# Kernel tuning notes

Measured on AMD Instinct MI355X. Metric: run time of the kernel, lower is better.

The kernel has to match this reference:

```python
import jax, jax.numpy as jnp
import numpy as np


def _c1(x, W, b):
    # 1x1 conv: W [out,in], x [B,in,H,W]
    return jnp.einsum('oi,bihw->bohw', W, x) + b[None, :, None, None]


def _c3(x, W, b):
    # 3x3 conv, stride 1, padding 1 (SAME)
    y = jax.lax.conv_general_dilated(x, W, (1, 1), 'SAME',
                                     dimension_numbers=('NCHW', 'OIHW', 'NCHW'))
    return y + b[None, :, None, None]


def _resize(x, h, w):
    # matches torch F.interpolate(mode='bilinear', align_corners=False)
    return jax.image.resize(x, (x.shape[0], x.shape[1], h, w), 'linear', antialias=False)


def setup_inputs() -> dict:
    key = jax.random.key(0)
    ks = jax.random.split(key, 20)
    B, C, H, W = 4, 64, 128, 128
    d = C // 8

    def n(k, shape, s=0.05):
        return jax.random.normal(k, shape, dtype=jnp.float32) * s

    z = lambda c: jnp.zeros((c,), jnp.float32)
    return {
        'x': jax.random.normal(ks[0], (B, C, H, W), dtype=jnp.float32),
        'mask': jax.random.normal(ks[1], (B, 64, H, W), dtype=jnp.float32),
        'Wq': n(ks[2], (d, C)), 'bq': z(d),
        'Wk': n(ks[3], (d, C)), 'bk': z(d),
        'Wv': n(ks[4], (C, C)), 'bv': z(C),
        'alpha1': jax.random.uniform(ks[5], (1,), dtype=jnp.float32),
        'alpha2': jax.random.uniform(ks[6], (1,), dtype=jnp.float32),
        'mq_w1': n(ks[7], (64, 64, 3, 3)), 'mq_b1': z(64),
        'mq_w2': n(ks[8], (d, 64)), 'mq_b2': z(d),
        'mk_w1': n(ks[9], (64, 64, 3, 3)), 'mk_b1': z(64),
        'mk_w2': n(ks[10], (d, 64)), 'mk_b2': z(d),
        'ca_w1': n(ks[11], (64, 64)), 'ca_b1': z(64),
        'ca_w2': n(ks[12], (64, 64)), 'ca_b2': z(64),
    }


def reference(x, mask, Wq, bq, Wk, bk, Wv, bv, alpha1, alpha2,
              mq_w1, mq_b1, mq_w2, mq_b2, mk_w1, mk_b1, mk_w2, mk_b2,
              ca_w1, ca_b1, ca_w2, ca_b2):
    B, C, H, W = x.shape
    h2, w2 = H // 2, W // 2
    N = h2 * w2

    mask_q = _c1(jax.nn.relu(_c3(mask, mq_w1, mq_b1)), mq_w2, mq_b2)
    mask_k = _c1(jax.nn.relu(_c3(mask, mk_w1, mk_b1)), mk_w2, mk_b2)
    xq = _c1(x, Wq, bq)  # [B, d, H, W]
    xk = _c1(x, Wk, bk)

    pq = mask_q * xq * alpha1 + xq * (1.0 - alpha1)
    pq = _resize(pq, h2, w2).reshape(B, -1, N)          # [B, d, N]
    pk = mask_k * xk * alpha2 + xk * (1.0 - alpha2)
    pk = _resize(pk, h2, w2).reshape(B, -1, N)          # [B, d, N]

    energy = jnp.einsum('bdn,bdm->bnm', pq, pk)         # [B, N, N]
    attn = jax.nn.softmax(energy, axis=-1)

    pv = _resize(_c1(x, Wv, bv), h2, w2).reshape(B, C, N)
    out = jnp.einsum('bcn,bmn->bcm', pv, attn)          # value @ attn^T
    out = out.reshape(B, C, h2, w2)
    out = _resize(out, H, W)
    out = _c1(jax.nn.relu(_c1(out, ca_w1, ca_b1)), ca_w2, ca_b2)
    return out + x
```

## Files before the change

kernel.cpp:

```cpp
#include <hip/hip_runtime.h>
#include <hip/hip_bf16.h>

typedef _Float16 half8 __attribute__((ext_vector_type(8)));
typedef _Float16 half4v __attribute__((ext_vector_type(4)));
typedef _Float16 half2v __attribute__((ext_vector_type(2)));
typedef __fp16 pkh2 __attribute__((ext_vector_type(2)));
typedef float f32x4 __attribute__((ext_vector_type(4)));

static __device__ __forceinline__ f32x4 mfma16(half8 a, half8 b, f32x4 c) {
    return __builtin_amdgcn_mfma_f32_16x16x32_f16(a, b, c, 0, 0, 0);
}

typedef const __attribute__((address_space(1))) unsigned int* gas_ptr;
typedef __attribute__((address_space(3))) unsigned int* las_ptr;
static __device__ __forceinline__ void gload16(const void* g, void* l) {
    __builtin_amdgcn_global_load_lds((gas_ptr)g, (las_ptr)l, 16, 0, 0);
}

static __device__ __forceinline__ half2v cvt2(float a, float b) {
    pkh2 t = __builtin_amdgcn_cvt_pkrtz(a, b);
    return __builtin_bit_cast(half2v, t);
}
static __device__ __forceinline__ half8 pk8(f32x4 a, f32x4 b) {
    half2v x0 = cvt2(a[0], a[1]);
    half2v x1 = cvt2(a[2], a[3]);
    half2v x2 = cvt2(b[0], b[1]);
    half2v x3 = cvt2(b[2], b[3]);
    half4v lo = __builtin_shufflevector(x0, x1, 0, 1, 2, 3);
    half4v hi = __builtin_shufflevector(x2, x3, 0, 1, 2, 3);
    return __builtin_shufflevector(lo, hi, 0, 1, 2, 3, 4, 5, 6, 7);
}
static __device__ __forceinline__ half4v pk4(f32x4 a) {
    half2v x0 = cvt2(a[0], a[1]);
    half2v x1 = cvt2(a[2], a[3]);
    return __builtin_shufflevector(x0, x1, 0, 1, 2, 3);
}

#define WS_APCONV   0u
#define WS_APW2S    147456u
#define WS_APCA     151552u
#define WS_APW2K4   159744u
#define WS_PACKED   196608u
#define WS_MASKQ    8849408u
#define WS_MASKK    10946560u
#define WS_Q16      13043712u
#define WS_K16      13305856u
#define WS_V16      13568000u
#define WS_ZB       15665152u
#define WS_PACC8    17762304u
#define WS_PML8     34539520u
#define WS_END8     35063808u
#define WS_PACC4    WS_PACKED
#define WS_PML4     WS_MASKQ

__global__ __launch_bounds__(256) void prep_pack_kernel(
    const float* __restrict__ mask,
    const float* __restrict__ mqw1, const float* __restrict__ mkw1,
    const float* __restrict__ mqw2, const float* __restrict__ mkw2,
    const float* __restrict__ caw1, const float* __restrict__ caw2,
    _Float16* __restrict__ packed,
    _Float16* __restrict__ ApackConv, _Float16* __restrict__ ApackW2s,
    _Float16* __restrict__ ApackCA, _Float16* __restrict__ ApackW2K4)
{
    int tid = threadIdx.x;
    if (blockIdx.z < 4) {
        int ich = blockIdx.y, b = blockIdx.z;
        _Float16* Pb = packed + ((size_t)b * 8 + ich) * 130 * 130 * 8;
        if (blockIdx.x < 2) {
            for (int p = blockIdx.x * 260 + tid; p < (int)(blockIdx.x + 1) * 260; p += 256) {
                int row, col;
                if (p < 130)      { row = 0;       col = p; }
                else if (p < 260) { row = 129;     col = p - 130; }
                else if (p < 390) { row = p - 260; col = 0; }
                else              { row = p - 390; col = 129; }
                half8 z = {};
                *(half8*)(Pb + ((size_t)row * 130 + col) * 8) = z;
            }
        }
        int x = tid & 127;
        int sy = blockIdx.x * 2 + (tid >> 7);
        half8 v;
#pragma unroll
        for (int cc = 0; cc < 8; cc++)
            v[cc] = (_Float16)mask[(((size_t)(b * 64 + ich * 8 + cc)) * 128 + sy) * 128 + x];
        *(half8*)(Pb + (((size_t)(sy + 1)) * 130 + (x + 1)) * 8) = v;
        return;
    }
    int tid0 = (blockIdx.y * 64 + blockIdx.x) * 256 + tid;
    const int stride = 512 * 256;
    for (int idx = tid0; idx < 73728; idx += stride) {
        int j = idx & 7, lane = (idx >> 3) & 63, mf = (idx >> 9) & 3;
        int ks18 = idx >> 11;
        int br = ks18 / 18, kstep = ks18 % 18;
        int oc = mf * 16 + (lane & 15);
        int g = lane >> 4;
        int k = kstep * 32 + g * 8 + j;
        int tap = k >> 6, ic = k & 63;
        int dy = tap / 3, dx = tap - dy * 3;
        const float* w1 = br ? mkw1 : mqw1;
        ApackConv[idx] = (_Float16)w1[((oc * 64 + ic) * 3 + dy) * 3 + dx];
    }
    for (int idx = tid0; idx < 2048; idx += stride) {
        int j = idx & 7, lane = (idx >> 3) & 63;
        int f = (idx >> 9) & 1, br = idx >> 10;
        int dc = lane & 15, g = lane >> 4;
        int kap = 16 * (2 * f + (j >> 2)) + 4 * g + (j & 3);
        const float* w2 = br ? mkw2 : mqw2;
        ApackW2s[idx] = (_Float16)((dc < 8) ? w2[dc * 64 + kap] : 0.f);
    }
    for (int idx = tid0; idx < 4096; idx += stride) {
        int j = idx & 7, lane = (idx >> 3) & 63, mf = (idx >> 9) & 3, f = idx >> 11;
        int cp = mf * 16 + (lane & 15), g = lane >> 4;
        int kap = 16 * (2 * f + (j >> 2)) + 4 * g + (j & 3);
        ApackCA[idx] = (_Float16)caw1[cp * 64 + kap];
    }
    for (int idx = tid0; idx < 4096; idx += stride) {
        int j = idx & 7, lane = (idx >> 3) & 63, mf = (idx >> 9) & 3, f = idx >> 11;
        int cc = mf * 16 + (lane & 15), g = lane >> 4;
        int cpk = f * 32 + g * 8 + j;
        ApackW2K4[idx] = (_Float16)caw2[cc * 64 + cpk];
    }
}

__global__ __launch_bounds__(256) void conv_mask_kernel(
    const _Float16* __restrict__ packed,
    const _Float16* __restrict__ ApackConv,
    const _Float16* __restrict__ ApackW2s,
    const float* __restrict__ mqb1, const float* __restrict__ mqb2,
    const float* __restrict__ mkb1, const float* __restrict__ mkb2,
    float* __restrict__ maskq, float* __restrict__ maskk)
{
    __shared__ __align__(16) _Float16 S[8 * 4 * 72 * 8];
    int tid = threadIdx.x;
    int lane = tid & 63, w = tid >> 6;
    int x0 = blockIdx.x * 64;
    int y0 = blockIdx.y * 2;
    int b = blockIdx.z;
    int row = w & 1, br = w >> 1;
    int q = lane & 15, g = lane >> 4;

    const _Float16* Pb = packed + (size_t)b * 8 * 130 * 130 * 8;
#pragma unroll
    for (int i = 0; i < 8; i++) {
        int p = w * 8 + i;
        int ich = p >> 2, pr = p & 3;
        const _Float16* src = Pb + (((size_t)ich * 130 + (y0 + pr)) * 130 + x0) * 8;
        _Float16* dst = S + ((ich * 4 + pr) * 72) * 8;
        gload16(src + lane * 8, dst);
        if (lane < 8) gload16(src + (64 + lane) * 8, dst + 64 * 8);
    }
    __syncthreads();

    const _Float16* Ab = ApackConv + br * 36864;
    f32x4 acc[4][4] = {};
    for (int kstep = 0; kstep < 18; kstep++) {
        int tap = kstep >> 1;
        int dyv = tap / 3, dxv = tap - dyv * 3;
        int ich = (kstep & 1) * 4 + g;
        const _Float16* srow = S + ((ich * 4 + row + dyv) * 72 + q + dxv) * 8;
        half8 bf[4];
#pragma unroll
        for (int nf = 0; nf < 4; nf++)
            bf[nf] = *(const half8*)(srow + nf * 128);
        const _Float16* Ak = Ab + kstep * 2048 + lane * 8;
#pragma unroll
        for (int mf = 0; mf < 4; mf++) {
            half8 af = *(const half8*)(Ak + mf * 512);
#pragma unroll
            for (int nf = 0; nf < 4; nf++)
                acc[mf][nf] = mfma16(af, bf[nf], acc[mf][nf]);
        }
    }
    const float* b1p = br ? mkb1 : mqb1;
    const float* b2p = br ? mkb2 : mqb2;
    float* outp = br ? maskk : maskq;
    float b1v[16];
#pragma unroll
    for (int mf = 0; mf < 4; mf++)
#pragma unroll
        for (int r = 0; r < 4; r++) b1v[mf * 4 + r] = b1p[mf * 16 + g * 4 + r];
    f32x4 acc2[4] = {};
#pragma unroll
    for (int f = 0; f < 2; f++) {
        half8 a2 = *(const half8*)(ApackW2s + (br * 2 + f) * 512 + lane * 8);
#pragma unroll
        for (int nf = 0; nf < 4; nf++) {
            half8 b2f;
#pragma unroll
            for (int j = 0; j < 8; j++) {
                int mfj = 2 * f + (j >> 2), rj = j & 3;
                b2f[j] = (_Float16)fmaxf(acc[mfj][nf][rj] + b1v[mfj * 4 + rj], 0.f);
            }
            acc2[nf] = mfma16(a2, b2f, acc2[nf]);
        }
    }
    if (g < 2) {
        int y = y0 + row;
#pragma unroll
        for (int r = 0; r < 4; r++) {
            int dc = g * 4 + r;
            float bb = b2p[dc];
#pragma unroll
            for (int nf = 0; nf < 4; nf++)
                outp[((size_t)(b * 8 + dc) * 128 + y) * 128 + (x0 + nf * 16 + q)] =
                    acc2[nf][r] + bb;
        }
    }
}

__global__ __launch_bounds__(512) void proj_kernel(
    const float* __restrict__ xg,
    const float* __restrict__ maskq, const float* __restrict__ maskk,
    const float* __restrict__ Wq, const float* __restrict__ bq,
    const float* __restrict__ Wk, const float* __restrict__ bk,
    const float* __restrict__ Wv, const float* __restrict__ bv,
    const float* __restrict__ a1p, const float* __restrict__ a2p,
    _Float16* __restrict__ Qg, _Float16* __restrict__ Kg, _Float16* __restrict__ Vg)
{
    __shared__ float xr[16384];
    __shared__ float xw[4096];
    __shared__ float lWv[4096], lWq[512], lWk[512];
    int tid = threadIdx.x;
    int b = blockIdx.x >> 6, i = blockIdx.x & 63;

    for (int idx = tid; idx < 16384; idx += 512) {
        int ic = idx >> 8, rem = idx & 255;
        xr[idx] = xg[((size_t)(b * 64 + ic) * 128 + (2 * i + (rem >> 7))) * 128 + (rem & 127)];
    }
    for (int idx = tid; idx < 4096; idx += 512) lWv[idx] = Wv[idx];
    lWq[tid] = Wq[tid];
    lWk[tid] = Wk[tid];
    __syncthreads();
    for (int idx = tid; idx < 4096; idx += 512) {
        int ic = idx >> 6, j = idx & 63;
        const float* base = &xr[ic * 256 + 2 * j];
        xw[idx] = 0.25f * (base[0] + base[1] + base[128] + base[129]);
    }
    __syncthreads();

    if (tid < 256) {
        int c0 = tid >> 5;
        int j0 = (tid & 31) * 2;
        float acc0[8], acc1[8];
#pragma unroll
        for (int u = 0; u < 8; u++) { float bb = bv[c0 + 8 * u]; acc0[u] = bb; acc1[u] = bb; }
        for (int ic = 0; ic < 64; ic++) {
            float x0v = xw[ic * 64 + j0], x1v = xw[ic * 64 + j0 + 1];
#pragma unroll
            for (int u = 0; u < 8; u++) {
                float ww = lWv[(c0 + 8 * u) * 64 + ic];
                acc0[u] += ww * x0v; acc1[u] += ww * x1v;
            }
        }
        int f = j0 >> 5, gg = (j0 & 15) >> 2, hi = (j0 >> 4) & 1;
        int off = (f * 4 + gg) * 8 + (j0 & 3) + 4 * hi;
#pragma unroll
        for (int u = 0; u < 8; u++) {
            int c = c0 + 8 * u;
            _Float16* p = Vg + (size_t)(b * 64 + c) * 4096 + i * 64 + off;
            p[0] = (_Float16)acc0[u]; p[1] = (_Float16)acc1[u];
        }
    } else {
        int t = tid - 256;
        int branch = t >> 7;
        int ysel = t & 1;
        int j = (t >> 1) & 63;
        const float* W = branch ? lWk : lWq;
        const float* bias = branch ? bk : bq;
        float alpha = branch ? a2p[0] : a1p[0];
        const float* mq = branch ? maskk : maskq;
        _Float16* outg = branch ? Kg : Qg;
        int x0c = 2 * j, x1c = 2 * j + 1;
        float aq0[8], aq1[8];
#pragma unroll
        for (int dc = 0; dc < 8; dc++) { float bb = bias[dc]; aq0[dc] = bb; aq1[dc] = bb; }
        for (int ic = 0; ic < 64; ic++) {
            float xv0 = xr[ic * 256 + ysel * 128 + x0c];
            float xv1 = xr[ic * 256 + ysel * 128 + x1c];
#pragma unroll
            for (int dc = 0; dc < 8; dc++) {
                float ww = W[dc * 64 + ic];
                aq0[dc] += ww * xv0; aq1[dc] += ww * xv1;
            }
        }
        int yy = 2 * i + ysel;
        half8 vq;
#pragma unroll
        for (int dc = 0; dc < 8; dc++) {
            size_t mbase = ((size_t)(b * 8 + dc) * 128 + yy) * 128;
            float m0v = mq[mbase + x0c], m1v = mq[mbase + x1c];
            float s = aq0[dc] * (alpha * m0v + (1.f - alpha))
                    + aq1[dc] * (alpha * m1v + (1.f - alpha));
            s += __shfl_xor(s, 1);
            vq[dc] = (_Float16)(0.25f * s);
        }
        if (ysel == 0)
            *(half8*)(outg + ((size_t)b * 4096 + i * 64 + j) * 8) = vq;
    }
}

__global__ __launch_bounds__(512, 4) void attn_kernel(
    const _Float16* __restrict__ Qg, const _Float16* __restrict__ Kg,
    const _Float16* __restrict__ Vg, const _Float16* __restrict__ ApackCA,
    _Float16* __restrict__ pacc, float* __restrict__ pml,
    int bmask, int sshift, int bbase)
{
    __shared__ __align__(16) _Float16 Vlds[8 * 4096];
    __shared__ __align__(16) _Float16 Klds[8 * 512];
    int tid = threadIdx.x, lane = tid & 63, w = tid >> 6;
    int q = lane & 15, g = lane >> 4;
    int bid = blockIdx.x;
    int qt = bid & 15, b = bbase + ((bid >> 4) & bmask), s = bid >> sshift;

    const _Float16* Kb = Kg + ((size_t)b * 4096 + s * 512) * 8;
    const _Float16* Vbase = Vg + (size_t)b * 64 * 4096 + s * 512;

    {
        int cc = w * 8 + (lane >> 3);
        int chl = (lane & 7) ^ (cc & 7);
        const _Float16* src0 = Vbase + (size_t)cc * 4096 + chl * 8;
#pragma unroll
        for (int t = 0; t < 8; t++)
            gload16(src0 + t * 64, Vlds + t * 4096 + w * 512);
        gload16(Kb + (size_t)(w * 64 + lane) * 8, Klds + w * 512);
    }
    half8 qf0 = {}, qf1 = {};
    if (g == 0) {
        int qb = qt * 256 + w * 32 + q;
        half8 r0 = *(const half8*)(Qg + ((size_t)b * 4096 + qb) * 8);
        half8 r1 = *(const half8*)(Qg + ((size_t)b * 4096 + qb + 16) * 8);
#pragma unroll
        for (int j = 0; j < 8; j++) {
            qf0[j] = (_Float16)((float)r0[j] * 1.44269504f);
            qf1[j] = (_Float16)((float)r1[j] * 1.44269504f);
        }
    }
    __syncthreads();

    half8 ones;
#pragma unroll
    for (int j = 0; j < 8; j++) ones[j] = (_Float16)1.f;

    f32x4 acc0[4] = {}, acc1[4] = {};
    f32x4 accl0 = {}, accl1 = {};
    const f32x4 zero4 = {};

#pragma unroll 2
    for (int t = 0; t < 8; t++) {
        const _Float16* Kt = Klds + t * 512;
        half8 af0 = *(const half8*)(Kt + q * 8);
        half8 af1 = *(const half8*)(Kt + (16 + q) * 8);
        half8 af2 = *(const half8*)(Kt + (32 + q) * 8);
        half8 af3 = *(const half8*)(Kt + (48 + q) * 8);

        half8 pb00, pb01, pb10, pb11;
        {
            f32x4 s0 = mfma16(af0, qf0, zero4);
            f32x4 s1 = mfma16(af1, qf0, zero4);
            f32x4 s2 = mfma16(af2, qf0, zero4);
            f32x4 s3 = mfma16(af3, qf0, zero4);
            f32x4 e0, e1, e2, e3;
#pragma unroll
            for (int r = 0; r < 4; r++) {
                e0[r] = __builtin_amdgcn_exp2f(s0[r]);
                e1[r] = __builtin_amdgcn_exp2f(s1[r]);
                e2[r] = __builtin_amdgcn_exp2f(s2[r]);
                e3[r] = __builtin_amdgcn_exp2f(s3[r]);
            }
            pb00 = pk8(e0, e1); pb01 = pk8(e2, e3);
            accl0 = mfma16(ones, pb00, accl0);
            accl0 = mfma16(ones, pb01, accl0);
        }
        {
            f32x4 s0 = mfma16(af0, qf1, zero4);
            f32x4 s1 = mfma16(af1, qf1, zero4);
            f32x4 s2 = mfma16(af2, qf1, zero4);
            f32x4 s3 = mfma16(af3, qf1, zero4);
            f32x4 e0, e1, e2, e3;
#pragma unroll
            for (int r = 0; r < 4; r++) {
                e0[r] = __builtin_amdgcn_exp2f(s0[r]);
                e1[r] = __builtin_amdgcn_exp2f(s1[r]);
                e2[r] = __builtin_amdgcn_exp2f(s2[r]);
                e3[r] = __builtin_amdgcn_exp2f(s3[r]);
            }
            pb10 = pk8(e0, e1); pb11 = pk8(e2, e3);
            accl1 = mfma16(ones, pb10, accl1);
            accl1 = mfma16(ones, pb11, accl1);
        }
        const _Float16* Vl = Vlds + t * 4096;
        int sw = q & 7;
        __builtin_amdgcn_s_setprio(1);
#pragma unroll
        for (int mfc = 0; mfc < 4; mfc++) {
            const _Float16* vr = Vl + (mfc * 16 + q) * 64;
            half8 av0 = *(const half8*)(vr + (g ^ sw) * 8);
            half8 av1 = *(const half8*)(vr + ((4 + g) ^ sw) * 8);
            acc0[mfc] = mfma16(av0, pb00, acc0[mfc]);
            acc1[mfc] = mfma16(av0, pb10, acc1[mfc]);
            acc0[mfc] = mfma16(av1, pb01, acc0[mfc]);
            acc1[mfc] = mfma16(av1, pb11, acc1[mfc]);
        }
        __builtin_amdgcn_s_setprio(0);
    }

    half8 a3[8];
#pragma unroll
    for (int i = 0; i < 8; i++) a3[i] = *(const half8*)(ApackCA + i * 512 + lane * 8);
    {
        half8 ob0 = pk8(acc0[0], acc0[1]);
        half8 ob1 = pk8(acc0[2], acc0[3]);
        f32x4 z[4] = {};
#pragma unroll
        for (int mf2 = 0; mf2 < 4; mf2++) {
            z[mf2] = mfma16(a3[mf2], ob0, z[mf2]);
            z[mf2] = mfma16(a3[4 + mf2], ob1, z[mf2]);
        }
        size_t prow = ((size_t)bid * 256 + w * 32 + q) * 64;
#pragma unroll
        for (int mf2 = 0; mf2 < 4; mf2++)
            *(half4v*)(pacc + prow + mf2 * 16 + g * 4) = pk4(z[mf2]);
        if (g == 0) pml[bid * 256 + w * 32 + q] = accl0[0];
    }
    {
        half8 ob0 = pk8(acc1[0], acc1[1]);
        half8 ob1 = pk8(acc1[2], acc1[3]);
        f32x4 z[4] = {};
#pragma unroll
        for (int mf2 = 0; mf2 < 4; mf2++) {
            z[mf2] = mfma16(a3[mf2], ob0, z[mf2]);
            z[mf2] = mfma16(a3[4 + mf2], ob1, z[mf2]);
        }
        size_t prow = ((size_t)bid * 256 + w * 32 + 16 + q) * 64;
#pragma unroll
        for (int mf2 = 0; mf2 < 4; mf2++)
            *(half4v*)(pacc + prow + mf2 * 16 + g * 4) = pk4(z[mf2]);
        if (g == 0) pml[bid * 256 + w * 32 + 16 + q] = accl1[0];
    }
}

__global__ __launch_bounds__(256) void combine_kernel(
    const _Float16* __restrict__ pacc, const float* __restrict__ pml,
    const float* __restrict__ cb1, _Float16* __restrict__ zb,
    int tps, int bbase)
{
    int T = blockIdx.x * 256 + threadIdx.x;
    int e = T & 7, row = T >> 3;
    int brel = row >> 12, qg = row & 4095;
    int qt16 = qg >> 8, ql = qg & 255;
    int tb0 = brel * 16 + qt16;

    float sum[8] = {};
    float L = 0.f;
    for (int s = 0; s < 8; s++) {
        int tile = s * tps + tb0;
        half8 v = *(const half8*)(pacc + ((size_t)tile * 256 + ql) * 64 + e * 8);
#pragma unroll
        for (int i = 0; i < 8; i++) sum[i] += (float)v[i];
        L += pml[tile * 256 + ql];
    }
    float inv = 1.f / L;
    half8 o;
#pragma unroll
    for (int i = 0; i < 8; i++) o[i] = (_Float16)(sum[i] * inv + cb1[e * 8 + i]);
    *(half8*)(zb + ((size_t)(bbase + brel) * 4096 + qg) * 64 + e * 8) = o;
}

template <int FUSED>
__global__ __launch_bounds__(512) void post_kernel(
    const _Float16* __restrict__ zg,
    const _Float16* __restrict__ pacc, const float* __restrict__ pml,
    const float* __restrict__ cb1,
    const float* __restrict__ xg,
    const _Float16* __restrict__ ApackW2K4, const float* __restrict__ cb2,
    float* __restrict__ outg)
{
    __shared__ _Float16 zt[6 * 18 * 72];
    int tid = threadIdx.x, lane = tid & 63, w = tid >> 6;
    int x0 = blockIdx.x * 32, y0 = blockIdx.y * 8, b = blockIdx.z;
    int r0 = 4 * (int)blockIdx.y - 1;
    int cbs = 16 * (int)blockIdx.x - 1;
    const _Float16* zgb = zg + (size_t)b * 4096 * 64;
    for (int idx = tid; idx < 864; idx += 512) {
        int rowi = idx >> 3, ch = idx & 7;
        int r = rowi / 18, col = rowi - r * 18;
        int zr = min(max(r0 + r, 0), 63);
        int zc = min(max(cbs + col, 0), 63);
        if constexpr (FUSED) {
            int zq = zr * 64 + zc;
            int tb = b * 16 + (zq >> 8);
            int ql = zq & 255;
            float sum[8] = {};
            float L = 0.f;
#pragma unroll
            for (int s = 0; s < 8; s++) {
                int tile = s * 64 + tb;
                half8 v = *(const half8*)(pacc + ((size_t)tile * 256 + ql) * 64 + ch * 8);
#pragma unroll
                for (int i2 = 0; i2 < 8; i2++) sum[i2] += (float)v[i2];
                L += pml[tile * 256 + ql];
            }
            float inv = 1.f / L;
            half8 o;
#pragma unroll
            for (int i2 = 0; i2 < 8; i2++) o[i2] = (_Float16)(sum[i2] * inv + cb1[ch * 8 + i2]);
            *(half8*)&zt[(r * 18 + col) * 72 + ch * 8] = o;
        } else {
            half8 v = *(const half8*)(zgb + ((size_t)(zr * 64 + zc)) * 64 + ch * 8);
            *(half8*)&zt[(r * 18 + col) * 72 + ch * 8] = v;
        }
    }
    __syncthreads();

    int q = lane & 15, g = lane >> 4;
    int y = y0 + w;
    int ra = (w >> 1) + (w & 1);
    float wyA = (w & 1) ? 0.75f : 0.25f;
    float wyB = 1.f - wyA;
    f32x4 acc[4][2] = {};
#pragma unroll
    for (int f = 0; f < 2; f++) {
        half8 a[4];
#pragma unroll
        for (int mf = 0; mf < 4; mf++)
            a[mf] = *(const half8*)(ApackW2K4 + (f * 4 + mf) * 512 + lane * 8);
#pragma unroll
        for (int nf = 0; nf < 2; nf++) {
            int pxl = nf * 16 + q;
            int ca = (pxl >> 1) + (pxl & 1);
            float wxA = (pxl & 1) ? 0.75f : 0.25f;
            float wxB = 1.f - wxA;
            half8 bfrag;
#pragma unroll
            for (int qd = 0; qd < 2; qd++) {
                int cpb = f * 32 + g * 8 + qd * 4;
                const _Float16* z00 = &zt[(ra * 18 + ca) * 72 + cpb];
                half4v h00 = *(const half4v*)z00;
                half4v h01 = *(const half4v*)(z00 + 72);
                half4v h10 = *(const half4v*)(z00 + 18 * 72);
                half4v h11 = *(const half4v*)(z00 + 18 * 72 + 72);
#pragma unroll
                for (int e = 0; e < 4; e++) {
                    float zu = ((float)h00[e] * wxA + (float)h01[e] * wxB) * wyA
                             + ((float)h10[e] * wxA + (float)h11[e] * wxB) * wyB;
                    bfrag[qd * 4 + e] = (_Float16)fmaxf(zu, 0.f);
                }
            }
#pragma unroll
            for (int mf = 0; mf < 4; mf++) acc[mf][nf] = mfma16(a[mf], bfrag, acc[mf][nf]);
        }
    }
#pragma unroll
    for (int mf = 0; mf < 4; mf++)
#pragma unroll
        for (int r = 0; r < 4; r++) {
            int c = mf * 16 + g * 4 + r;
            float bb = cb2[c];
#pragma unroll
            for (int nf = 0; nf < 2; nf++) {
                size_t oidx = ((size_t)(b * 64 + c) * 128 + y) * 128 + x0 + nf * 16 + q;
                outg[oidx] = acc[mf][nf][r] + bb + xg[oidx];
            }
        }
}

extern "C" void kernel_launch(void* const* d_in, const int* in_sizes, int n_in,
                              void* d_out, int out_size, void* d_ws, size_t ws_size,
                              hipStream_t stream)
{
    const float* x    = (const float*)d_in[0];
    const float* mask = (const float*)d_in[1];
    const float* Wq   = (const float*)d_in[2];
    const float* bq   = (const float*)d_in[3];
    const float* Wk   = (const float*)d_in[4];
    const float* bk   = (const float*)d_in[5];
    const float* Wv   = (const float*)d_in[6];
    const float* bv   = (const float*)d_in[7];
    const float* a1   = (const float*)d_in[8];
    const float* a2   = (const float*)d_in[9];
    const float* mqw1 = (const float*)d_in[10];
    const float* mqb1 = (const float*)d_in[11];
    const float* mqw2 = (const float*)d_in[12];
    const float* mqb2 = (const float*)d_in[13];
    const float* mkw1 = (const float*)d_in[14];
    const float* mkb1 = (const float*)d_in[15];
    const float* mkw2 = (const float*)d_in[16];
    const float* mkb2 = (const float*)d_in[17];
    const float* caw1 = (const float*)d_in[18];
    const float* cab1 = (const float*)d_in[19];
    const float* caw2 = (const float*)d_in[20];
    const float* cab2 = (const float*)d_in[21];

    char* ws = (char*)d_ws;
    _Float16* ApackConv = (_Float16*)(ws + WS_APCONV);
    _Float16* ApackW2s  = (_Float16*)(ws + WS_APW2S);
    _Float16* ApackCA   = (_Float16*)(ws + WS_APCA);
    _Float16* ApackW2K4 = (_Float16*)(ws + WS_APW2K4);
    _Float16* packed    = (_Float16*)(ws + WS_PACKED);
    float*    maskq     = (float*)(ws + WS_MASKQ);
    float*    maskk     = (float*)(ws + WS_MASKK);
    _Float16* Qg16      = (_Float16*)(ws + WS_Q16);
    _Float16* Kg16      = (_Float16*)(ws + WS_K16);
    _Float16* Vb        = (_Float16*)(ws + WS_V16);
    _Float16* zb        = (_Float16*)(ws + WS_ZB);

    prep_pack_kernel<<<dim3(64, 8, 5), dim3(256), 0, stream>>>(
        mask, mqw1, mkw1, mqw2, mkw2, caw1, caw2,
        packed, ApackConv, ApackW2s, ApackCA, ApackW2K4);
    conv_mask_kernel<<<dim3(2, 64, 4), dim3(256), 0, stream>>>(
        packed, ApackConv, ApackW2s, mqb1, mqb2, mkb1, mkb2, maskq, maskk);
    proj_kernel<<<dim3(256), dim3(512), 0, stream>>>(
        x, maskq, maskk, Wq, bq, Wk, bk, Wv, bv, a1, a2, Qg16, Kg16, Vb);

    bool big = (ws_size >= (size_t)WS_END8);
    if (big) {
        _Float16* pacc = (_Float16*)(ws + WS_PACC8);
        float*    pml  = (float*)(ws + WS_PML8);
        attn_kernel<<<dim3(512), dim3(512), 0, stream>>>(
            Qg16, Kg16, Vb, ApackCA, pacc, pml, 3, 6, 0);
        post_kernel<1><<<dim3(4, 16, 4), dim3(512), 0, stream>>>(
            zb, pacc, pml, cab1, x, ApackW2K4, cab2, (float*)d_out);
    } else {
        _Float16* pacc = (_Float16*)(ws + WS_PACC4);
        float*    pml  = (float*)(ws + WS_PML4);
        for (int bbase = 0; bbase < 4; bbase += 2) {
            attn_kernel<<<dim3(256), dim3(512), 0, stream>>>(
                Qg16, Kg16, Vb, ApackCA, pacc, pml, 1, 5, bbase);
            combine_kernel<<<dim3(256), dim3(256), 0, stream>>>(pacc, pml, cab1, zb, 32, bbase);
        }
        post_kernel<0><<<dim3(4, 16, 4), dim3(512), 0, stream>>>(
            zb, nullptr, nullptr, cab1, x, ApackW2K4, cab2, (float*)d_out);
    }
}
```

Measured before the change: 79.21 us.

## Halve attention query tile per block, unfuse combine, store masks in fp16

Each attention block now handles 128 query rows (16 per wave) instead of 256, which doubles the grid to 1024 blocks and roughly halves per-wave accumulator registers. The combine of split-K partials moves out of post_kernel into a separate combine_kernel in the big-workspace path, and post_kernel loses its fused template variant. The mask_q/mask_k intermediates are written and read as fp16 instead of fp32, cutting that traffic in half. The smaller tile means each block reloads the same K/V tiles into LDS for fewer queries, so K/V loading grows, and the extra launch adds overhead.

```diff
diff --git a/kernel.cpp b/kernel.cpp
--- a/kernel.cpp
+++ b/kernel.cpp
@@ -128,7 +128,7 @@
     const _Float16* __restrict__ ApackW2s,
     const float* __restrict__ mqb1, const float* __restrict__ mqb2,
     const float* __restrict__ mkb1, const float* __restrict__ mkb2,
-    float* __restrict__ maskq, float* __restrict__ maskk)
+    _Float16* __restrict__ maskq, _Float16* __restrict__ maskk)
 {
     __shared__ __align__(16) _Float16 S[8 * 4 * 72 * 8];
     int tid = threadIdx.x;
@@ -173,7 +173,7 @@
     }
     const float* b1p = br ? mkb1 : mqb1;
     const float* b2p = br ? mkb2 : mqb2;
-    float* outp = br ? maskk : maskq;
+    _Float16* outp = br ? maskk : maskq;
     float b1v[16];
 #pragma unroll
     for (int mf = 0; mf < 4; mf++)
@@ -203,14 +203,14 @@
 #pragma unroll
             for (int nf = 0; nf < 4; nf++)
                 outp[((size_t)(b * 8 + dc) * 128 + y) * 128 + (x0 + nf * 16 + q)] =
-                    acc2[nf][r] + bb;
+                    (_Float16)(acc2[nf][r] + bb);
         }
     }
 }
 
 __global__ __launch_bounds__(512) void proj_kernel(
     const float* __restrict__ xg,
-    const float* __restrict__ maskq, const float* __restrict__ maskk,
+    const _Float16* __restrict__ maskq, const _Float16* __restrict__ maskk,
     const float* __restrict__ Wq, const float* __restrict__ bq,
     const float* __restrict__ Wk, const float* __restrict__ bk,
     const float* __restrict__ Wv, const float* __restrict__ bv,
@@ -268,7 +268,7 @@
         const float* W = branch ? lWk : lWq;
         const float* bias = branch ? bk : bq;
         float alpha = branch ? a2p[0] : a1p[0];
-        const float* mq = branch ? maskk : maskq;
+        const _Float16* mq = branch ? maskk : maskq;
         _Float16* outg = branch ? Kg : Qg;
         int x0c = 2 * j, x1c = 2 * j + 1;
         float aq0[8], aq1[8];
@@ -288,7 +288,7 @@
 #pragma unroll
         for (int dc = 0; dc < 8; dc++) {
             size_t mbase = ((size_t)(b * 8 + dc) * 128 + yy) * 128;
-            float m0v = mq[mbase + x0c], m1v = mq[mbase + x1c];
+            float m0v = (float)mq[mbase + x0c], m1v = (float)mq[mbase + x1c];
             float s = aq0[dc] * (alpha * m0v + (1.f - alpha))
                     + aq1[dc] * (alpha * m1v + (1.f - alpha));
             s += __shfl_xor(s, 1);
@@ -310,7 +310,7 @@
     int tid = threadIdx.x, lane = tid & 63, w = tid >> 6;
     int q = lane & 15, g = lane >> 4;
     int bid = blockIdx.x;
-    int qt = bid & 15, b = bbase + ((bid >> 4) & bmask), s = bid >> sshift;
+    int qt = bid & 31, b = bbase + ((bid >> 5) & bmask), s = bid >> sshift;
 
     const _Float16* Kb = Kg + ((size_t)b * 4096 + s * 512) * 8;
     const _Float16* Vbase = Vg + (size_t)b * 64 * 4096 + s * 512;
@@ -324,16 +324,13 @@
             gload16(src0 + t * 64, Vlds + t * 4096 + w * 512);
         gload16(Kb + (size_t)(w * 64 + lane) * 8, Klds + w * 512);
     }
-    half8 qf0 = {}, qf1 = {};
+    half8 qf = {};
     if (g == 0) {
-        int qb = qt * 256 + w * 32 + q;
+        int qb = qt * 128 + w * 16 + q;
         half8 r0 = *(const half8*)(Qg + ((size_t)b * 4096 + qb) * 8);
-        half8 r1 = *(const half8*)(Qg + ((size_t)b * 4096 + qb + 16) * 8);
-#pragma unroll
-        for (int j = 0; j < 8; j++) {
-            qf0[j] = (_Float16)((float)r0[j] * 1.44269504f);
-            qf1[j] = (_Float16)((float)r1[j] * 1.44269504f);
-        }
+#pragma unroll
+        for (int j = 0; j < 8; j++)
+            qf[j] = (_Float16)((float)r0[j] * 1.44269504f);
     }
     __syncthreads();
 
@@ -341,11 +338,11 @@
 #pragma unroll
     for (int j = 0; j < 8; j++) ones[j] = (_Float16)1.f;
 
-    f32x4 acc0[4] = {}, acc1[4] = {};
-    f32x4 accl0 = {}, accl1 = {};
+    f32x4 acc[4] = {};
+    f32x4 accl = {};
     const f32x4 zero4 = {};
 
-#pragma unroll 2
+#pragma unroll 1
     for (int t = 0; t < 8; t++) {
         const _Float16* Kt = Klds + t * 512;
         half8 af0 = *(const half8*)(Kt + q * 8);
@@ -353,41 +350,22 @@
         half8 af2 = *(const half8*)(Kt + (32 + q) * 8);
         half8 af3 = *(const half8*)(Kt + (48 + q) * 8);
 
-        half8 pb00, pb01, pb10, pb11;
-        {
-            f32x4 s0 = mfma16(af0, qf0, zero4);
-            f32x4 s1 = mfma16(af1, qf0, zero4);
-            f32x4 s2 = mfma16(af2, qf0, zero4);
-            f32x4 s3 = mfma16(af3, qf0, zero4);
-            f32x4 e0, e1, e2, e3;
-#pragma unroll
-            for (int r = 0; r < 4; r++) {
-                e0[r] = __builtin_amdgcn_exp2f(s0[r]);
-                e1[r] = __builtin_amdgcn_exp2f(s1[r]);
-                e2[r] = __builtin_amdgcn_exp2f(s2[r]);
-                e3[r] = __builtin_amdgcn_exp2f(s3[r]);
-            }
-            pb00 = pk8(e0, e1); pb01 = pk8(e2, e3);
-            accl0 = mfma16(ones, pb00, accl0);
-            accl0 = mfma16(ones, pb01, accl0);
-        }
-        {
-            f32x4 s0 = mfma16(af0, qf1, zero4);
-            f32x4 s1 = mfma16(af1, qf1, zero4);
-            f32x4 s2 = mfma16(af2, qf1, zero4);
-            f32x4 s3 = mfma16(af3, qf1, zero4);
-            f32x4 e0, e1, e2, e3;
-#pragma unroll
-            for (int r = 0; r < 4; r++) {
-                e0[r] = __builtin_amdgcn_exp2f(s0[r]);
-                e1[r] = __builtin_amdgcn_exp2f(s1[r]);
-                e2[r] = __builtin_amdgcn_exp2f(s2[r]);
-                e3[r] = __builtin_amdgcn_exp2f(s3[r]);
-            }
-            pb10 = pk8(e0, e1); pb11 = pk8(e2, e3);
-            accl1 = mfma16(ones, pb10, accl1);
-            accl1 = mfma16(ones, pb11, accl1);
-        }
+        f32x4 s0 = mfma16(af0, qf, zero4);
+        f32x4 s1 = mfma16(af1, qf, zero4);
+        f32x4 s2 = mfma16(af2, qf, zero4);
+        f32x4 s3 = mfma16(af3, qf, zero4);
+        f32x4 e0, e1, e2, e3;
+#pragma unroll
+        for (int r = 0; r < 4; r++) {
+            e0[r] = __builtin_amdgcn_exp2f(s0[r]);
+            e1[r] = __builtin_amdgcn_exp2f(s1[r]);
+            e2[r] = __builtin_amdgcn_exp2f(s2[r]);
+            e3[r] = __builtin_amdgcn_exp2f(s3[r]);
+        }
+        half8 pb0 = pk8(e0, e1), pb1 = pk8(e2, e3);
+        accl = mfma16(ones, pb0, accl);
+        accl = mfma16(ones, pb1, accl);
+
         const _Float16* Vl = Vlds + t * 4096;
         int sw = q & 7;
         __builtin_amdgcn_s_setprio(1);
@@ -396,47 +374,27 @@
             const _Float16* vr = Vl + (mfc * 16 + q) * 64;
             half8 av0 = *(const half8*)(vr + (g ^ sw) * 8);
             half8 av1 = *(const half8*)(vr + ((4 + g) ^ sw) * 8);
-            acc0[mfc] = mfma16(av0, pb00, acc0[mfc]);
-            acc1[mfc] = mfma16(av0, pb10, acc1[mfc]);
-            acc0[mfc] = mfma16(av1, pb01, acc0[mfc]);
-            acc1[mfc] = mfma16(av1, pb11, acc1[mfc]);
+            acc[mfc] = mfma16(av0, pb0, acc[mfc]);
+            acc[mfc] = mfma16(av1, pb1, acc[mfc]);
         }
         __builtin_amdgcn_s_setprio(0);
     }
 
-    half8 a3[8];
-#pragma unroll
-    for (int i = 0; i < 8; i++) a3[i] = *(const half8*)(ApackCA + i * 512 + lane * 8);
-    {
-        half8 ob0 = pk8(acc0[0], acc0[1]);
-        half8 ob1 = pk8(acc0[2], acc0[3]);
-        f32x4 z[4] = {};
-#pragma unroll
-        for (int mf2 = 0; mf2 < 4; mf2++) {
-            z[mf2] = mfma16(a3[mf2], ob0, z[mf2]);
-            z[mf2] = mfma16(a3[4 + mf2], ob1, z[mf2]);
-        }
-        size_t prow = ((size_t)bid * 256 + w * 32 + q) * 64;
-#pragma unroll
-        for (int mf2 = 0; mf2 < 4; mf2++)
-            *(half4v*)(pacc + prow + mf2 * 16 + g * 4) = pk4(z[mf2]);
-        if (g == 0) pml[bid * 256 + w * 32 + q] = accl0[0];
-    }
-    {
-        half8 ob0 = pk8(acc1[0], acc1[1]);
-        half8 ob1 = pk8(acc1[2], acc1[3]);
-        f32x4 z[4] = {};
-#pragma unroll
-        for (int mf2 = 0; mf2 < 4; mf2++) {
-            z[mf2] = mfma16(a3[mf2], ob0, z[mf2]);
-            z[mf2] = mfma16(a3[4 + mf2], ob1, z[mf2]);
-        }
-        size_t prow = ((size_t)bid * 256 + w * 32 + 16 + q) * 64;
-#pragma unroll
-        for (int mf2 = 0; mf2 < 4; mf2++)
-            *(half4v*)(pacc + prow + mf2 * 16 + g * 4) = pk4(z[mf2]);
-        if (g == 0) pml[bid * 256 + w * 32 + 16 + q] = accl1[0];
-    }
+    half8 ob0 = pk8(acc[0], acc[1]);
+    half8 ob1 = pk8(acc[2], acc[3]);
+    f32x4 z[4] = {};
+#pragma unroll
+    for (int mf2 = 0; mf2 < 4; mf2++) {
+        half8 a30 = *(const half8*)(ApackCA + mf2 * 512 + lane * 8);
+        half8 a31 = *(const half8*)(ApackCA + (4 + mf2) * 512 + lane * 8);
+        z[mf2] = mfma16(a30, ob0, z[mf2]);
+        z[mf2] = mfma16(a31, ob1, z[mf2]);
+    }
+    size_t prow = ((size_t)bid * 128 + w * 16 + q) * 64;
+#pragma unroll
+    for (int mf2 = 0; mf2 < 4; mf2++)
+        *(half4v*)(pacc + prow + mf2 * 16 + g * 4) = pk4(z[mf2]);
+    if (g == 0) pml[bid * 128 + w * 16 + q] = accl[0];
 }
 
 __global__ __launch_bounds__(256) void combine_kernel(
@@ -447,17 +405,17 @@
     int T = blockIdx.x * 256 + threadIdx.x;
     int e = T & 7, row = T >> 3;
     int brel = row >> 12, qg = row & 4095;
-    int qt16 = qg >> 8, ql = qg & 255;
-    int tb0 = brel * 16 + qt16;
+    int qt = qg >> 7, ql = qg & 127;
+    int tb0 = brel * 32 + qt;
 
     float sum[8] = {};
     float L = 0.f;
     for (int s = 0; s < 8; s++) {
         int tile = s * tps + tb0;
-        half8 v = *(const half8*)(pacc + ((size_t)tile * 256 + ql) * 64 + e * 8);
+        half8 v = *(const half8*)(pacc + ((size_t)tile * 128 + ql) * 64 + e * 8);
 #pragma unroll
         for (int i = 0; i < 8; i++) sum[i] += (float)v[i];
-        L += pml[tile * 256 + ql];
+        L += pml[tile * 128 + ql];
     }
     float inv = 1.f / L;
     half8 o;
@@ -466,11 +424,8 @@
     *(half8*)(zb + ((size_t)(bbase + brel) * 4096 + qg) * 64 + e * 8) = o;
 }
 
-template <int FUSED>
 __global__ __launch_bounds__(512) void post_kernel(
     const _Float16* __restrict__ zg,
-    const _Float16* __restrict__ pacc, const float* __restrict__ pml,
-    const float* __restrict__ cb1,
     const float* __restrict__ xg,
     const _Float16* __restrict__ ApackW2K4, const float* __restrict__ cb2,
     float* __restrict__ outg)
@@ -486,29 +441,8 @@
         int r = rowi / 18, col = rowi - r * 18;
         int zr = min(max(r0 + r, 0), 63);
         int zc = min(max(cbs + col, 0), 63);
-        if constexpr (FUSED) {
-            int zq = zr * 64 + zc;
-            int tb = b * 16 + (zq >> 8);
-            int ql = zq & 255;
-            float sum[8] = {};
-            float L = 0.f;
-#pragma unroll
-            for (int s = 0; s < 8; s++) {
-                int tile = s * 64 + tb;
-                half8 v = *(const half8*)(pacc + ((size_t)tile * 256 + ql) * 64 + ch * 8);
-#pragma unroll
-                for (int i2 = 0; i2 < 8; i2++) sum[i2] += (float)v[i2];
-                L += pml[tile * 256 + ql];
-            }
-            float inv = 1.f / L;
-            half8 o;
-#pragma unroll
-            for (int i2 = 0; i2 < 8; i2++) o[i2] = (_Float16)(sum[i2] * inv + cb1[ch * 8 + i2]);
-            *(half8*)&zt[(r * 18 + col) * 72 + ch * 8] = o;
-        } else {
-            half8 v = *(const half8*)(zgb + ((size_t)(zr * 64 + zc)) * 64 + ch * 8);
-            *(half8*)&zt[(r * 18 + col) * 72 + ch * 8] = v;
-        }
+        half8 v = *(const half8*)(zgb + ((size_t)(zr * 64 + zc)) * 64 + ch * 8);
+        *(half8*)&zt[(r * 18 + col) * 72 + ch * 8] = v;
     }
     __syncthreads();
 
@@ -597,8 +531,8 @@
     _Float16* ApackCA   = (_Float16*)(ws + WS_APCA);
     _Float16* ApackW2K4 = (_Float16*)(ws + WS_APW2K4);
     _Float16* packed    = (_Float16*)(ws + WS_PACKED);
-    float*    maskq     = (float*)(ws + WS_MASKQ);
-    float*    maskk     = (float*)(ws + WS_MASKK);
+    _Float16* maskq     = (_Float16*)(ws + WS_MASKQ);
+    _Float16* maskk     = (_Float16*)(ws + WS_MASKK);
     _Float16* Qg16      = (_Float16*)(ws + WS_Q16);
     _Float16* Kg16      = (_Float16*)(ws + WS_K16);
     _Float16* Vb        = (_Float16*)(ws + WS_V16);
@@ -616,19 +550,18 @@
     if (big) {
         _Float16* pacc = (_Float16*)(ws + WS_PACC8);
         float*    pml  = (float*)(ws + WS_PML8);
-        attn_kernel<<<dim3(512), dim3(512), 0, stream>>>(
-            Qg16, Kg16, Vb, ApackCA, pacc, pml, 3, 6, 0);
-        post_kernel<1><<<dim3(4, 16, 4), dim3(512), 0, stream>>>(
-            zb, pacc, pml, cab1, x, ApackW2K4, cab2, (float*)d_out);
+        attn_kernel<<<dim3(1024), dim3(512), 0, stream>>>(
+            Qg16, Kg16, Vb, ApackCA, pacc, pml, 3, 7, 0);
+        combine_kernel<<<dim3(512), dim3(256), 0, stream>>>(pacc, pml, cab1, zb, 128, 0);
     } else {
         _Float16* pacc = (_Float16*)(ws + WS_PACC4);
         float*    pml  = (float*)(ws + WS_PML4);
         for (int bbase = 0; bbase < 4; bbase += 2) {
-            attn_kernel<<<dim3(256), dim3(512), 0, stream>>>(
-                Qg16, Kg16, Vb, ApackCA, pacc, pml, 1, 5, bbase);
-            combine_kernel<<<dim3(256), dim3(256), 0, stream>>>(pacc, pml, cab1, zb, 32, bbase);
-        }
-        post_kernel<0><<<dim3(4, 16, 4), dim3(512), 0, stream>>>(
-            zb, nullptr, nullptr, cab1, x, ApackW2K4, cab2, (float*)d_out);
-    }
-}
+            attn_kernel<<<dim3(512), dim3(512), 0, stream>>>(
+                Qg16, Kg16, Vb, ApackCA, pacc, pml, 1, 6, bbase);
+            combine_kernel<<<dim3(256), dim3(256), 0, stream>>>(pacc, pml, cab1, zb, 64, bbase);
+        }
+    }
+    post_kernel<<<dim3(4, 16, 4), dim3(512), 0, stream>>>(
+        zb, x, ApackW2K4, cab2, (float*)d_out);
+}
```

Result: no change. 80.61 us (+1.8%).

## Move V projection into conv kernel blocks and shrink Q/K projection kernel

Applied to the files above, without the earlier changes.

The V projection (2x2 average then 64x64 1x1 conv) moves out of the projection kernel into extra blocks of the mask-conv launch (grid z from 4 to 6), so it runs concurrently with the mask convolution. The remaining Q/K projection kernel drops to 256 threads and stores the x tile in fp16 in shared memory to cut LDS use. The mask_q/mask_k intermediates are stored as fp16 instead of fp32, halving their traffic. The cost is reduced precision in x and the masks for Q/K, plus extra global reads of x in the V blocks.

```diff
diff --git a/kernel.cpp b/kernel.cpp
--- a/kernel.cpp
+++ b/kernel.cpp
@@ -122,16 +122,67 @@
     }
 }
 
-__global__ __launch_bounds__(256) void conv_mask_kernel(
+__global__ __launch_bounds__(256) void conv_vproj_kernel(
     const _Float16* __restrict__ packed,
     const _Float16* __restrict__ ApackConv,
     const _Float16* __restrict__ ApackW2s,
     const float* __restrict__ mqb1, const float* __restrict__ mqb2,
     const float* __restrict__ mkb1, const float* __restrict__ mkb2,
-    float* __restrict__ maskq, float* __restrict__ maskk)
+    const float* __restrict__ xg,
+    const float* __restrict__ Wv, const float* __restrict__ bv,
+    _Float16* __restrict__ maskq, _Float16* __restrict__ maskk,
+    _Float16* __restrict__ Vg)
 {
-    __shared__ __align__(16) _Float16 S[8 * 4 * 72 * 8];
+    __shared__ __align__(16) char shmem[36864];
     int tid = threadIdx.x;
+
+    if (blockIdx.z >= 4) {
+        float* xw  = (float*)shmem;
+        float* lWv = (float*)(shmem + 16384);
+        lWv = (float*)(shmem + 8192);
+        int vb = (blockIdx.z - 4) * 128 + blockIdx.y * 2 + blockIdx.x;
+        int b = vb >> 6, i = vb & 63;
+        for (int idx = tid; idx < 2048; idx += 256) {
+            int ic = idx >> 5, j = idx & 31;
+            const float* px = xg + ((size_t)(b * 64 + ic) * 128 + 2 * i) * 128 + 2 * j;
+            xw[idx] = 0.25f * (px[0] + px[1] + px[128] + px[129]);
+        }
+        for (int idx = tid; idx < 4096; idx += 256) lWv[idx] = Wv[idx];
+        __syncthreads();
+        for (int jh = 0; jh < 2; jh++) {
+            if (jh == 1) {
+                __syncthreads();
+                for (int idx = tid; idx < 2048; idx += 256) {
+                    int ic = idx >> 5, j = idx & 31;
+                    const float* px = xg + ((size_t)(b * 64 + ic) * 128 + 2 * i) * 128 + 2 * (32 + j);
+                    xw[idx] = 0.25f * (px[0] + px[1] + px[128] + px[129]);
+                }
+                __syncthreads();
+            }
+            int c0 = tid >> 5;
+            int jl = tid & 31;
+            float acc0[8];
+#pragma unroll
+            for (int u = 0; u < 8; u++) acc0[u] = bv[c0 + 8 * u];
+            for (int ic = 0; ic < 64; ic++) {
+                float xv = xw[ic * 32 + jl];
+#pragma unroll
+                for (int u = 0; u < 8; u++)
+                    acc0[u] += lWv[(c0 + 8 * u) * 64 + ic] * xv;
+            }
+            int j0 = jh * 32 + jl;
+            int f = j0 >> 5, gg = (j0 & 15) >> 2, hi = (j0 >> 4) & 1;
+            int off = (f * 4 + gg) * 8 + (j0 & 3) + 4 * hi;
+#pragma unroll
+            for (int u = 0; u < 8; u++) {
+                int c = c0 + 8 * u;
+                Vg[(size_t)(b * 64 + c) * 4096 + i * 64 + off] = (_Float16)acc0[u];
+            }
+        }
+        return;
+    }
+
+    _Float16* S = (_Float16*)shmem;
     int lane = tid & 63, w = tid >> 6;
     int x0 = blockIdx.x * 64;
     int y0 = blockIdx.y * 2;
@@ -173,7 +224,7 @@
     }
     const float* b1p = br ? mkb1 : mqb1;
     const float* b2p = br ? mkb2 : mqb2;
-    float* outp = br ? maskk : maskq;
+    _Float16* outp = br ? maskk : maskq;
     float b1v[16];
 #pragma unroll
     for (int mf = 0; mf < 4; mf++)
@@ -203,100 +254,69 @@
 #pragma unroll
             for (int nf = 0; nf < 4; nf++)
                 outp[((size_t)(b * 8 + dc) * 128 + y) * 128 + (x0 + nf * 16 + q)] =
-                    acc2[nf][r] + bb;
-        }
-    }
-}
-
-__global__ __launch_bounds__(512) void proj_kernel(
+                    (_Float16)(acc2[nf][r] + bb);
+        }
+    }
+}
+
+__global__ __launch_bounds__(256) void qkproj_kernel(
     const float* __restrict__ xg,
-    const float* __restrict__ maskq, const float* __restrict__ maskk,
+    const _Float16* __restrict__ maskq, const _Float16* __restrict__ maskk,
     const float* __restrict__ Wq, const float* __restrict__ bq,
     const float* __restrict__ Wk, const float* __restrict__ bk,
-    const float* __restrict__ Wv, const float* __restrict__ bv,
     const float* __restrict__ a1p, const float* __restrict__ a2p,
-    _Float16* __restrict__ Qg, _Float16* __restrict__ Kg, _Float16* __restrict__ Vg)
+    _Float16* __restrict__ Qg, _Float16* __restrict__ Kg)
 {
-    __shared__ float xr[16384];
-    __shared__ float xw[4096];
-    __shared__ float lWv[4096], lWq[512], lWk[512];
+    __shared__ _Float16 xr[16384];
+    __shared__ float lWq[512], lWk[512];
     int tid = threadIdx.x;
     int b = blockIdx.x >> 6, i = blockIdx.x & 63;
 
-    for (int idx = tid; idx < 16384; idx += 512) {
+    for (int idx = tid; idx < 16384; idx += 256) {
         int ic = idx >> 8, rem = idx & 255;
-        xr[idx] = xg[((size_t)(b * 64 + ic) * 128 + (2 * i + (rem >> 7))) * 128 + (rem & 127)];
-    }
-    for (int idx = tid; idx < 4096; idx += 512) lWv[idx] = Wv[idx];
-    lWq[tid] = Wq[tid];
+        xr[idx] = (_Float16)xg[((size_t)(b * 64 + ic) * 128 + (2 * i + (rem >> 7))) * 128 + (rem & 127)];
+    }
+    lWq[tid] = Wq[tid]; lWq[tid] = Wq[tid];
+    lWq[tid + 256] = Wq[tid + 256];
     lWk[tid] = Wk[tid];
+    lWk[tid + 256] = Wk[tid + 256];
     __syncthreads();
-    for (int idx = tid; idx < 4096; idx += 512) {
-        int ic = idx >> 6, j = idx & 63;
-        const float* base = &xr[ic * 256 + 2 * j];
-        xw[idx] = 0.25f * (base[0] + base[1] + base[128] + base[129]);
-    }
-    __syncthreads();
-
-    if (tid < 256) {
-        int c0 = tid >> 5;
-        int j0 = (tid & 31) * 2;
-        float acc0[8], acc1[8];
-#pragma unroll
-        for (int u = 0; u < 8; u++) { float bb = bv[c0 + 8 * u]; acc0[u] = bb; acc1[u] = bb; }
-        for (int ic = 0; ic < 64; ic++) {
-            float x0v = xw[ic * 64 + j0], x1v = xw[ic * 64 + j0 + 1];
-#pragma unroll
-            for (int u = 0; u < 8; u++) {
-                float ww = lWv[(c0 + 8 * u) * 64 + ic];
-                acc0[u] += ww * x0v; acc1[u] += ww * x1v;
-            }
-        }
-        int f = j0 >> 5, gg = (j0 & 15) >> 2, hi = (j0 >> 4) & 1;
-        int off = (f * 4 + gg) * 8 + (j0 & 3) + 4 * hi;
-#pragma unroll
-        for (int u = 0; u < 8; u++) {
-            int c = c0 + 8 * u;
-            _Float16* p = Vg + (size_t)(b * 64 + c) * 4096 + i * 64 + off;
-            p[0] = (_Float16)acc0[u]; p[1] = (_Float16)acc1[u];
-        }
-    } else {
-        int t = tid - 256;
-        int branch = t >> 7;
-        int ysel = t & 1;
-        int j = (t >> 1) & 63;
-        const float* W = branch ? lWk : lWq;
-        const float* bias = branch ? bk : bq;
-        float alpha = branch ? a2p[0] : a1p[0];
-        const float* mq = branch ? maskk : maskq;
-        _Float16* outg = branch ? Kg : Qg;
-        int x0c = 2 * j, x1c = 2 * j + 1;
-        float aq0[8], aq1[8];
-#pragma unroll
-        for (int dc = 0; dc < 8; dc++) { float bb = bias[dc]; aq0[dc] = bb; aq1[dc] = bb; }
-        for (int ic = 0; ic < 64; ic++) {
-            float xv0 = xr[ic * 256 + ysel * 128 + x0c];
-            float xv1 = xr[ic * 256 + ysel * 128 + x1c];
-#pragma unroll
-            for (int dc = 0; dc < 8; dc++) {
-                float ww = W[dc * 64 + ic];
-                aq0[dc] += ww * xv0; aq1[dc] += ww * xv1;
-            }
-        }
-        int yy = 2 * i + ysel;
-        half8 vq;
+
+    int branch = tid >> 7;
+    int t = tid & 127;
+    int ysel = t & 1;
+    int j = (t >> 1) & 63;
+    const float* W = branch ? lWk : lWq;
+    const float* bias = branch ? bk : bq;
+    float alpha = branch ? a2p[0] : a1p[0];
+    const _Float16* mq = branch ? maskk : maskq;
+    _Float16* outg = branch ? Kg : Qg;
+    int x0c = 2 * j, x1c = 2 * j + 1;
+    float aq0[8], aq1[8];
+#pragma unroll
+    for (int dc = 0; dc < 8; dc++) { float bb = bias[dc]; aq0[dc] = bb; aq1[dc] = bb; }
+    for (int ic = 0; ic < 64; ic++) {
+        float xv0 = (float)xr[ic * 256 + ysel * 128 + x0c];
+        float xv1 = (float)xr[ic * 256 + ysel * 128 + x1c];
 #pragma unroll
         for (int dc = 0; dc < 8; dc++) {
-            size_t mbase = ((size_t)(b * 8 + dc) * 128 + yy) * 128;
-            float m0v = mq[mbase + x0c], m1v = mq[mbase + x1c];
-            float s = aq0[dc] * (alpha * m0v + (1.f - alpha))
-                    + aq1[dc] * (alpha * m1v + (1.f - alpha));
-            s += __shfl_xor(s, 1);
-            vq[dc] = (_Float16)(0.25f * s);
-        }
-        if (ysel == 0)
-            *(half8*)(outg + ((size_t)b * 4096 + i * 64 + j) * 8) = vq;
-    }
+            float ww = W[dc * 64 + ic];
+            aq0[dc] += ww * xv0; aq1[dc] += ww * xv1;
+        }
+    }
+    int yy = 2 * i + ysel;
+    half8 vq;
+#pragma unroll
+    for (int dc = 0; dc < 8; dc++) {
+        size_t mbase = ((size_t)(b * 8 + dc) * 128 + yy) * 128;
+        float m0v = (float)mq[mbase + x0c], m1v = (float)mq[mbase + x1c];
+        float s = aq0[dc] * (alpha * m0v + (1.f - alpha))
+                + aq1[dc] * (alpha * m1v + (1.f - alpha));
+        s += __shfl_xor(s, 1);
+        vq[dc] = (_Float16)(0.25f * s);
+    }
+    if (ysel == 0)
+        *(half8*)(outg + ((size_t)b * 4096 + i * 64 + j) * 8) = vq;
 }
 
 __global__ __launch_bounds__(512, 4) void attn_kernel(
@@ -597,8 +617,8 @@
     _Float16* ApackCA   = (_Float16*)(ws + WS_APCA);
     _Float16* ApackW2K4 = (_Float16*)(ws + WS_APW2K4);
     _Float16* packed    = (_Float16*)(ws + WS_PACKED);
-    float*    maskq     = (float*)(ws + WS_MASKQ);
-    float*    maskk     = (float*)(ws + WS_MASKK);
+    _Float16* maskq     = (_Float16*)(ws + WS_MASKQ);
+    _Float16* maskk     = (_Float16*)(ws + WS_MASKK);
     _Float16* Qg16      = (_Float16*)(ws + WS_Q16);
     _Float16* Kg16      = (_Float16*)(ws + WS_K16);
     _Float16* Vb        = (_Float16*)(ws + WS_V16);
@@ -607,10 +627,11 @@
     prep_pack_kernel<<<dim3(64, 8, 5), dim3(256), 0, stream>>>(
         mask, mqw1, mkw1, mqw2, mkw2, caw1, caw2,
         packed, ApackConv, ApackW2s, ApackCA, ApackW2K4);
-    conv_mask_kernel<<<dim3(2, 64, 4), dim3(256), 0, stream>>>(
-        packed, ApackConv, ApackW2s, mqb1, mqb2, mkb1, mkb2, maskq, maskk);
-    proj_kernel<<<dim3(256), dim3(512), 0, stream>>>(
-        x, maskq, maskk, Wq, bq, Wk, bk, Wv, bv, a1, a2, Qg16, Kg16, Vb);
+    conv_vproj_kernel<<<dim3(2, 64, 6), dim3(256), 0, stream>>>(
+        packed, ApackConv, ApackW2s, mqb1, mqb2, mkb1, mkb2,
+        x, Wv, bv, maskq, maskk, Vb);
+    qkproj_kernel<<<dim3(256), dim3(256), 0, stream>>>(
+        x, maskq, maskk, Wq, bq, Wk, bk, a1, a2, Qg16, Kg16);
 
     bool big = (ws_size >= (size_t)WS_END8);
     if (big) {
```

After: 87.91 us. 11.0% more time.

## Restructure mask conv: stage weights in LDS, one branch per block, fp16 mask outputs

Applied to the files above, without the earlier changes.

The 3x3 mask conv kernel now gives each block a single branch (q or k) and 4 output rows. The branch's packed conv weights are staged once into LDS instead of being read from global per k-step. The input row stride is padded from 72 to 73 pixels, apparently to reduce LDS bank conflicts, and the k-step loop is fully unrolled. Mask outputs are written and read as fp16 instead of fp32, halving that intermediate traffic, which costs some precision and raises LDS use per block (about 130 KB), lowering occupancy.

```diff
diff --git a/kernel.cpp b/kernel.cpp
--- a/kernel.cpp
+++ b/kernel.cpp
@@ -128,41 +128,48 @@
     const _Float16* __restrict__ ApackW2s,
     const float* __restrict__ mqb1, const float* __restrict__ mqb2,
     const float* __restrict__ mkb1, const float* __restrict__ mkb2,
-    float* __restrict__ maskq, float* __restrict__ maskk)
+    _Float16* __restrict__ maskq, _Float16* __restrict__ maskk)
 {
-    __shared__ __align__(16) _Float16 S[8 * 4 * 72 * 8];
+    __shared__ __align__(16) _Float16 A[36864];
+    __shared__ __align__(16) _Float16 S[28032];
     int tid = threadIdx.x;
     int lane = tid & 63, w = tid >> 6;
     int x0 = blockIdx.x * 64;
-    int y0 = blockIdx.y * 2;
-    int b = blockIdx.z;
-    int row = w & 1, br = w >> 1;
+    int y0 = blockIdx.y * 4;
+    int bz = blockIdx.z;
+    int b = bz >> 1, br = bz & 1;
     int q = lane & 15, g = lane >> 4;
 
+    const _Float16* Ag = ApackConv + br * 36864;
+#pragma unroll
+    for (int i = 0; i < 18; i++) {
+        int off = w * 9216 + i * 512;
+        gload16(Ag + off + lane * 8, A + off);
+    }
     const _Float16* Pb = packed + (size_t)b * 8 * 130 * 130 * 8;
 #pragma unroll
-    for (int i = 0; i < 8; i++) {
-        int p = w * 8 + i;
-        int ich = p >> 2, pr = p & 3;
+    for (int i = 0; i < 12; i++) {
+        int rr = w * 12 + i;
+        int ich = rr / 6, pr = rr - ich * 6;
         const _Float16* src = Pb + (((size_t)ich * 130 + (y0 + pr)) * 130 + x0) * 8;
-        _Float16* dst = S + ((ich * 4 + pr) * 72) * 8;
+        _Float16* dst = S + (ich * 6 + pr) * 584;
         gload16(src + lane * 8, dst);
-        if (lane < 8) gload16(src + (64 + lane) * 8, dst + 64 * 8);
+        if (lane < 8) gload16(src + (64 + lane) * 8, dst + 512);
     }
     __syncthreads();
 
-    const _Float16* Ab = ApackConv + br * 36864;
     f32x4 acc[4][4] = {};
+#pragma unroll
     for (int kstep = 0; kstep < 18; kstep++) {
         int tap = kstep >> 1;
         int dyv = tap / 3, dxv = tap - dyv * 3;
         int ich = (kstep & 1) * 4 + g;
-        const _Float16* srow = S + ((ich * 4 + row + dyv) * 72 + q + dxv) * 8;
+        const _Float16* srow = S + ((ich * 6 + w + dyv) * 73 + q + dxv) * 8;
         half8 bf[4];
 #pragma unroll
         for (int nf = 0; nf < 4; nf++)
             bf[nf] = *(const half8*)(srow + nf * 128);
-        const _Float16* Ak = Ab + kstep * 2048 + lane * 8;
+        const _Float16* Ak = A + kstep * 2048 + lane * 8;
 #pragma unroll
         for (int mf = 0; mf < 4; mf++) {
             half8 af = *(const half8*)(Ak + mf * 512);
@@ -173,7 +180,7 @@
     }
     const float* b1p = br ? mkb1 : mqb1;
     const float* b2p = br ? mkb2 : mqb2;
-    float* outp = br ? maskk : maskq;
+    _Float16* outp = br ? maskk : maskq;
     float b1v[16];
 #pragma unroll
     for (int mf = 0; mf < 4; mf++)
@@ -195,7 +202,7 @@
         }
     }
     if (g < 2) {
-        int y = y0 + row;
+        int y = y0 + w;
 #pragma unroll
         for (int r = 0; r < 4; r++) {
             int dc = g * 4 + r;
@@ -203,14 +210,14 @@
 #pragma unroll
             for (int nf = 0; nf < 4; nf++)
                 outp[((size_t)(b * 8 + dc) * 128 + y) * 128 + (x0 + nf * 16 + q)] =
-                    acc2[nf][r] + bb;
+                    (_Float16)(acc2[nf][r] + bb);
         }
     }
 }
 
 __global__ __launch_bounds__(512) void proj_kernel(
     const float* __restrict__ xg,
-    const float* __restrict__ maskq, const float* __restrict__ maskk,
+    const _Float16* __restrict__ maskq, const _Float16* __restrict__ maskk,
     const float* __restrict__ Wq, const float* __restrict__ bq,
     const float* __restrict__ Wk, const float* __restrict__ bk,
     const float* __restrict__ Wv, const float* __restrict__ bv,
@@ -268,7 +275,7 @@
         const float* W = branch ? lWk : lWq;
         const float* bias = branch ? bk : bq;
         float alpha = branch ? a2p[0] : a1p[0];
-        const float* mq = branch ? maskk : maskq;
+        const _Float16* mq = branch ? maskk : maskq;
         _Float16* outg = branch ? Kg : Qg;
         int x0c = 2 * j, x1c = 2 * j + 1;
         float aq0[8], aq1[8];
@@ -288,7 +295,7 @@
 #pragma unroll
         for (int dc = 0; dc < 8; dc++) {
             size_t mbase = ((size_t)(b * 8 + dc) * 128 + yy) * 128;
-            float m0v = mq[mbase + x0c], m1v = mq[mbase + x1c];
+            float m0v = (float)mq[mbase + x0c], m1v = (float)mq[mbase + x1c];
             float s = aq0[dc] * (alpha * m0v + (1.f - alpha))
                     + aq1[dc] * (alpha * m1v + (1.f - alpha));
             s += __shfl_xor(s, 1);
@@ -597,8 +604,8 @@
     _Float16* ApackCA   = (_Float16*)(ws + WS_APCA);
     _Float16* ApackW2K4 = (_Float16*)(ws + WS_APW2K4);
     _Float16* packed    = (_Float16*)(ws + WS_PACKED);
-    float*    maskq     = (float*)(ws + WS_MASKQ);
-    float*    maskk     = (float*)(ws + WS_MASKK);
+    _Float16* maskq     = (_Float16*)(ws + WS_MASKQ);
+    _Float16* maskk     = (_Float16*)(ws + WS_MASKK);
     _Float16* Qg16      = (_Float16*)(ws + WS_Q16);
     _Float16* Kg16      = (_Float16*)(ws + WS_K16);
     _Float16* Vb        = (_Float16*)(ws + WS_V16);
@@ -607,7 +614,7 @@
     prep_pack_kernel<<<dim3(64, 8, 5), dim3(256), 0, stream>>>(
         mask, mqw1, mkw1, mqw2, mkw2, caw1, caw2,
         packed, ApackConv, ApackW2s, ApackCA, ApackW2K4);
-    conv_mask_kernel<<<dim3(2, 64, 4), dim3(256), 0, stream>>>(
+    conv_mask_kernel<<<dim3(2, 32, 8), dim3(256), 0, stream>>>(
         packed, ApackConv, ApackW2s, mqb1, mqb2, mkb1, mkb2, maskq, maskk);
     proj_kernel<<<dim3(256), dim3(512), 0, stream>>>(
         x, maskq, maskk, Wq, bq, Wk, bk, Wv, bv, a1, a2, Qg16, Kg16, Vb);
```

After: 65.35 us. 17.5% less time.
